# Optimization experiments

Measured on AMD Instinct MI355X. Metric: run time of the kernel, lower is better.

The kernel has to match this reference:

```python
import jax, jax.numpy as jnp
import numpy as np

ACT_BIT = 8
WEIGHT_BIT = 8
BIAS_BIT = 32
EPS = 1e-8


def _sym_scale(sat_max, bit):
    # symmetric_linear_quantization_params: scale = clamp(sat, 1e-8) / (2^(b-1)-1)
    n = 2 ** (bit - 1) - 1
    return jnp.maximum(sat_max, EPS) / n


def _sym_quant(x, scale, bit):
    # SymmetricQuantFunction: round(x/scale) clamped to [-2^(b-1), 2^(b-1)-1]
    n = 2 ** (bit - 1) - 1
    return jnp.clip(jnp.round(x / scale), -n - 1, n)


def setup_inputs() -> dict:
    key = jax.random.key(0)
    kx, kw, kb = jax.random.split(key, 3)
    B, S, D_IN, D_OUT = 4, 2048, 4096, 4096
    x = jax.random.normal(kx, (B, S, D_IN), dtype=jnp.float32)
    W = jax.random.normal(kw, (D_OUT, D_IN), dtype=jnp.float32) * 0.02
    b = jax.random.normal(kb, (D_OUT,), dtype=jnp.float32) * 0.02
    return {"x": x, "W": W, "b": b}


def reference(x, W, b):
    # --- QuantAct (per-tensor symmetric int8, min/max from x itself) ---
    x_min, x_max = x.min(), x.max()
    act_scale = _sym_scale(jnp.maximum(jnp.abs(x_min), jnp.abs(x_max)), ACT_BIT)
    x_int = _sym_quant(x, act_scale, ACT_BIT)  # [B,S,Din], int values in fp32

    # --- QuantLinearBase (per-tensor symmetric int8 weight, int32 bias) ---
    w_sat = jnp.maximum(jnp.abs(W.min()), jnp.abs(W.max()))
    w_scale = _sym_scale(w_sat, WEIGHT_BIT)
    w_int = _sym_quant(W, w_scale, WEIGHT_BIT)  # [Dout,Din]

    bias_scale = act_scale * w_scale
    n32 = 2 ** (BIAS_BIT - 1) - 1
    b_int = jnp.clip(jnp.round(b / bias_scale), -n32 - 1, n32)  # [Dout]

    # integer GEMM + bias, then rescale by act_scale * w_scale
    out_int = jnp.einsum("bsi,oi->bso", x_int, w_int) + b_int
    return out_int * bias_scale
```

## Files before the change

kernel.cpp:

```cpp
#include <hip/hip_runtime.h>
#include <cstdint>
#include <cstddef>


typedef int v4i __attribute__((ext_vector_type(4)));

__device__ __forceinline__ void async_copy16(const void* g, void* s) {
  __builtin_amdgcn_global_load_lds(
      (const __attribute__((address_space(1))) void*)g,
      (__attribute__((address_space(3))) void*)s, 16, 0, 0);
}

__device__ __forceinline__ float block_max(float m) {
  __shared__ float smax[4];
#pragma unroll
  for (int off = 32; off > 0; off >>= 1)
    m = fmaxf(m, __shfl_down(m, off, 64));
  if ((threadIdx.x & 63) == 0) smax[threadIdx.x >> 6] = m;
  __syncthreads();
  return fmaxf(fmaxf(smax[0], smax[1]), fmaxf(smax[2], smax[3]));
}

#define NBX 1024
#define NBW 512

__global__ __launch_bounds__(256) void absmax_partial_kernel(
    const float4* __restrict__ x, int xn4, const float4* __restrict__ w,
    int wn4, float* __restrict__ px, float* __restrict__ pw) {
  const float4* src;
  float* dst;
  int n4, bid, nb;
  if (blockIdx.x < NBX) {
    src = x; n4 = xn4; dst = px; bid = blockIdx.x; nb = NBX;
  } else {
    src = w; n4 = wn4; dst = pw; bid = blockIdx.x - NBX; nb = NBW;
  }
  float m = 0.0f;
  for (int i = bid * 256 + threadIdx.x; i < n4; i += nb * 256) {
    float4 v = src[i];
    m = fmaxf(m, fmaxf(fmaxf(fabsf(v.x), fabsf(v.y)),
                       fmaxf(fabsf(v.z), fabsf(v.w))));
  }
  m = block_max(m);
  if (threadIdx.x == 0) dst[bid] = m;
}

__global__ __launch_bounds__(256) void absmax_final_kernel(
    const float* __restrict__ px, const float* __restrict__ pw,
    float* __restrict__ sat) {
  const float* src = (blockIdx.x == 0) ? px : pw;
  const int n = (blockIdx.x == 0) ? NBX : NBW;
  float m = 0.0f;
  for (int i = threadIdx.x; i < n; i += 256) m = fmaxf(m, src[i]);
  m = block_max(m);
  if (threadIdx.x == 0) {
    sat[blockIdx.x] = m;
    sat[2 + blockIdx.x] = 127.0f / fmaxf(m, 1e-8f);
  }
}

__device__ __forceinline__ int pack4(float4 v, float inv) {
  int a = (int)fminf(fmaxf(rintf(v.x * inv), -128.0f), 127.0f);
  int b = (int)fminf(fmaxf(rintf(v.y * inv), -128.0f), 127.0f);
  int c = (int)fminf(fmaxf(rintf(v.z * inv), -128.0f), 127.0f);
  int d = (int)fminf(fmaxf(rintf(v.w * inv), -128.0f), 127.0f);
  return (a & 255) | ((b & 255) << 8) | ((c & 255) << 16) | ((d & 255) << 24);
}

#define QNB 2048

__global__ __launch_bounds__(256) void quant_fused_kernel(
    const float4* __restrict__ x, int xn16, const float4* __restrict__ w,
    int wn16, const float* __restrict__ sat, int4* __restrict__ xq,
    int4* __restrict__ wq) {
  const float invx = sat[2];
  const float invw = sat[3];
  const int nth = QNB * 256;
  const int t = blockIdx.x * 256 + threadIdx.x;
  for (int u = t; u < xn16; u += nth) {
    const float4* p = x + (size_t)u * 4;
    int4 o;
    o.x = pack4(p[0], invx);
    o.y = pack4(p[1], invx);
    o.z = pack4(p[2], invx);
    o.w = pack4(p[3], invx);
    xq[u] = o;
  }
  for (int u = t; u < wn16; u += nth) {
    const float4* p = w + (size_t)u * 4;
    int4 o;
    o.x = pack4(p[0], invw);
    o.y = pack4(p[1], invw);
    o.z = pack4(p[2], invw);
    o.w = pack4(p[3], invw);
    wq[u] = o;
  }
}

__global__ __launch_bounds__(256) void i8_gemm_kernel(
    const signed char* __restrict__ Aq, const signed char* __restrict__ Bq,
    const float* __restrict__ bias, const float* __restrict__ sat,
    float* __restrict__ out, int M, int N, int K) {
  __shared__ signed char Als[128 * 128];
  __shared__ signed char Bls[128 * 128];

  const int tid = threadIdx.x;
  const int lane = tid & 63;
  const int wave = tid >> 6;
  const int wm = (wave & 1) * 64;
  const int wn = (wave >> 1) * 64;

  const int nwg = gridDim.x * gridDim.y;
  int bid = blockIdx.y * gridDim.x + blockIdx.x;
  if ((nwg & 7) == 0) bid = (bid & 7) * (nwg >> 3) + (bid >> 3);
  const int N0 = (bid % gridDim.x) * 128;
  const int M0 = (bid / gridDim.x) * 128;

  const int srow = tid >> 3;
  const int sb = tid & 7;
  const int cg = sb ^ (srow & 7);
  const signed char* Ag = Aq + (size_t)(M0 + srow) * K + cg * 16;
  const signed char* Bg = Bq + (size_t)(N0 + srow) * K + cg * 16;
  signed char* AlsP = &Als[srow * 128 + sb * 16];
  signed char* BlsP = &Bls[srow * 128 + sb * 16];

  const int r15 = lane & 15;
  const int rx = r15 & 7;
  const int q4 = lane >> 4;
  const int kb0 = ((q4) ^ rx) * 16;
  const int kb1 = ((4 + q4) ^ rx) * 16;

  v4i acc[4][4] = {};

  for (int kt = 0; kt < K; kt += 128) {
    __syncthreads();
#pragma unroll
    for (int r = 0; r < 4; ++r) {
      async_copy16(Ag + kt + (size_t)(32 * r) * K, AlsP + 32 * r * 128);
      async_copy16(Bg + kt + (size_t)(32 * r) * K, BlsP + 32 * r * 128);
    }
    __syncthreads();

#pragma unroll
    for (int ks = 0; ks < 2; ++ks) {
      const int kb = ks ? kb1 : kb0;
      v4i af[4], bf[4];
#pragma unroll
      for (int t = 0; t < 4; ++t) {
        af[t] = *(const v4i*)&Als[(wm + t * 16 + r15) * 128 + kb];
        bf[t] = *(const v4i*)&Bls[(wn + t * 16 + r15) * 128 + kb];
      }
#pragma unroll
      for (int tm = 0; tm < 4; ++tm)
#pragma unroll
        for (int tn = 0; tn < 4; ++tn)
          acc[tm][tn] = __builtin_amdgcn_mfma_i32_16x16x64_i8(
              af[tm], bf[tn], acc[tm][tn], 0, 0, 0);
    }
  }

  const float act_s = fmaxf(sat[0], 1e-8f) / 127.0f;
  const float w_s = fmaxf(sat[1], 1e-8f) / 127.0f;
  const float bscale = act_s * w_s;

#pragma unroll
  for (int tn = 0; tn < 4; ++tn) {
    const int col = N0 + wn + tn * 16 + r15;
    const float fb = rintf(bias[col] / bscale);
#pragma unroll
    for (int tm = 0; tm < 4; ++tm) {
      const int row0 = M0 + wm + tm * 16 + q4 * 4;
#pragma unroll
      for (int r = 0; r < 4; ++r) {
        out[(size_t)(row0 + r) * N + col] =
            ((float)acc[tm][tn][r] + fb) * bscale;
      }
    }
  }
}

extern "C" void kernel_launch(void* const* d_in, const int* in_sizes, int n_in,
                              void* d_out, int out_size, void* d_ws,
                              size_t ws_size, hipStream_t stream) {
  const float* x = (const float*)d_in[0];
  const float* W = (const float*)d_in[1];
  const float* b = (const float*)d_in[2];
  float* out = (float*)d_out;

  const int Dout = in_sizes[2];
  const int K = in_sizes[1] / Dout;
  const int M = in_sizes[0] / K;
  const int N = Dout;

  float* sat = (float*)d_ws;
  float* px = sat + 16;
  float* pw = px + NBX;
  signed char* xq = (signed char*)d_ws + 8192;
  signed char* wq = xq + (size_t)M * K;

  const int xn4 = in_sizes[0] / 4;
  const int wn4 = in_sizes[1] / 4;

  absmax_partial_kernel<<<NBX + NBW, 256, 0, stream>>>(
      (const float4*)x, xn4, (const float4*)W, wn4, px, pw);
  absmax_final_kernel<<<2, 256, 0, stream>>>(px, pw, sat);
  quant_fused_kernel<<<QNB, 256, 0, stream>>>(
      (const float4*)x, xn4 / 4, (const float4*)W, wn4 / 4, sat, (int4*)xq,
      (int4*)wq);

  dim3 grid(N / 128, M / 128);
  i8_gemm_kernel<<<grid, 256, 0, stream>>>(xq, wq, b, sat, out, M, N, K);
}
```

Before: 493.1 us.

## Rewrite int8 GEMM with 256x256 tiles and 4-stage async LDS pipeline

The int8 GEMM moves from 128x128 tiles with 4 waves and a single-buffered load/compute loop to 256x256 tiles with 8 waves, a 4-deep ring of 64-wide K slices in LDS, and a rotation-based swizzle. Global-to-LDS copies for future tiles are interleaved between two MFMA phases, with explicit vmcnt waits, barriers and setprio, so memory latency overlaps with compute. This raises reuse per loaded byte and hides load latency. In exchange it uses 128KB of LDS and more accumulator registers, which limits occupancy to one block per CU.

```diff
diff --git a/kernel.cpp b/kernel.cpp
--- a/kernel.cpp
+++ b/kernel.cpp
@@ -97,66 +97,111 @@
   }
 }
 
-__global__ __launch_bounds__(256) void i8_gemm_kernel(
+__global__ __launch_bounds__(512, 2) void i8_gemm_kernel(
     const signed char* __restrict__ Aq, const signed char* __restrict__ Bq,
     const float* __restrict__ bias, const float* __restrict__ sat,
     float* __restrict__ out, int M, int N, int K) {
-  __shared__ signed char Als[128 * 128];
-  __shared__ signed char Bls[128 * 128];
+  __shared__ signed char lds[4][2][256 * 64];
 
   const int tid = threadIdx.x;
   const int lane = tid & 63;
-  const int wave = tid >> 6;
-  const int wm = (wave & 1) * 64;
-  const int wn = (wave >> 1) * 64;
+  const int wid = tid >> 6;
+  const int wr = wid >> 2;
+  const int wc = wid & 3;
+  const int r15 = lane & 15;
+  const int q4 = lane >> 4;
 
   const int nwg = gridDim.x * gridDim.y;
   int bid = blockIdx.y * gridDim.x + blockIdx.x;
   if ((nwg & 7) == 0) bid = (bid & 7) * (nwg >> 3) + (bid >> 3);
-  const int N0 = (bid % gridDim.x) * 128;
-  const int M0 = (bid / gridDim.x) * 128;
-
-  const int srow = tid >> 3;
-  const int sb = tid & 7;
-  const int cg = sb ^ (srow & 7);
+  const int N0 = (bid % gridDim.x) * 256;
+  const int M0 = (bid / gridDim.x) * 256;
+
+  const int srow = tid >> 2;
+  const int sb = tid & 3;
+  const int cg = (sb - ((srow >> 1) & 3)) & 3;
   const signed char* Ag = Aq + (size_t)(M0 + srow) * K + cg * 16;
   const signed char* Bg = Bq + (size_t)(N0 + srow) * K + cg * 16;
-  signed char* AlsP = &Als[srow * 128 + sb * 16];
-  signed char* BlsP = &Bls[srow * 128 + sb * 16];
-
-  const int r15 = lane & 15;
-  const int rx = r15 & 7;
-  const int q4 = lane >> 4;
-  const int kb0 = ((q4) ^ rx) * 16;
-  const int kb1 = ((4 + q4) ^ rx) * 16;
-
-  v4i acc[4][4] = {};
-
-  for (int kt = 0; kt < K; kt += 128) {
-    __syncthreads();
-#pragma unroll
-    for (int r = 0; r < 4; ++r) {
-      async_copy16(Ag + kt + (size_t)(32 * r) * K, AlsP + 32 * r * 128);
-      async_copy16(Bg + kt + (size_t)(32 * r) * K, BlsP + 32 * r * 128);
-    }
-    __syncthreads();
-
-#pragma unroll
-    for (int ks = 0; ks < 2; ++ks) {
-      const int kb = ks ? kb1 : kb0;
-      v4i af[4], bf[4];
-#pragma unroll
-      for (int t = 0; t < 4; ++t) {
-        af[t] = *(const v4i*)&Als[(wm + t * 16 + r15) * 128 + kb];
-        bf[t] = *(const v4i*)&Bls[(wn + t * 16 + r15) * 128 + kb];
-      }
-#pragma unroll
-      for (int tm = 0; tm < 4; ++tm)
-#pragma unroll
-        for (int tn = 0; tn < 4; ++tn)
-          acc[tm][tn] = __builtin_amdgcn_mfma_i32_16x16x64_i8(
-              af[tm], bf[tn], acc[tm][tn], 0, 0, 0);
-    }
+  const int d0 = srow * 64 + sb * 16;
+  const size_t rstep = (size_t)128 * K;
+
+  const int kboff = ((q4 + ((r15 >> 1) & 3)) & 3) * 16;
+
+  v4i acc[8][4] = {};
+  const int nt = K >> 6;
+
+  for (int T = 0; T < 3; ++T) {
+    const size_t ko = (size_t)T << 6;
+    signed char* bA = &lds[T & 3][0][0];
+    signed char* bB = &lds[T & 3][1][0];
+    async_copy16(Ag + ko, bA + d0);
+    async_copy16(Ag + ko + rstep, bA + d0 + 8192);
+    async_copy16(Bg + ko, bB + d0);
+    async_copy16(Bg + ko + rstep, bB + d0 + 8192);
+  }
+  asm volatile("s_waitcnt vmcnt(8)" ::: "memory");
+  __builtin_amdgcn_s_barrier();
+
+  for (int t = 0; t < nt; ++t) {
+    const signed char* bA = &lds[t & 3][0][0];
+    const signed char* bB = &lds[t & 3][1][0];
+    const int tp = t + 3;
+    const bool st = tp < nt;
+    signed char* sA = &lds[tp & 3][0][0];
+    signed char* sB = &lds[tp & 3][1][0];
+    const size_t ko = (size_t)tp << 6;
+
+    v4i af[4], bf[4];
+
+#pragma unroll
+    for (int f = 0; f < 4; ++f) {
+      af[f] = *(const v4i*)(bA + (wr * 128 + f * 16 + r15) * 64 + kboff);
+      bf[f] = *(const v4i*)(bB + (wc * 64 + f * 16 + r15) * 64 + kboff);
+    }
+    if (st) {
+      async_copy16(Ag + ko, sA + d0);
+      async_copy16(Ag + ko + rstep, sA + d0 + 8192);
+    }
+    __builtin_amdgcn_s_barrier();
+    asm volatile("s_waitcnt lgkmcnt(0)" ::: "memory");
+    __builtin_amdgcn_sched_barrier(0);
+    __builtin_amdgcn_s_setprio(1);
+#pragma unroll
+    for (int fm = 0; fm < 4; ++fm)
+#pragma unroll
+      for (int fn = 0; fn < 4; ++fn)
+        acc[fm][fn] = __builtin_amdgcn_mfma_i32_16x16x64_i8(
+            af[fm], bf[fn], acc[fm][fn], 0, 0, 0);
+    __builtin_amdgcn_s_setprio(0);
+    __builtin_amdgcn_s_barrier();
+
+#pragma unroll
+    for (int f = 0; f < 4; ++f) {
+      af[f] = *(const v4i*)(bA + (wr * 128 + 64 + f * 16 + r15) * 64 + kboff);
+    }
+    if (st) {
+      async_copy16(Bg + ko, sB + d0);
+      async_copy16(Bg + ko + rstep, sB + d0 + 8192);
+    }
+    __builtin_amdgcn_s_barrier();
+    asm volatile("s_waitcnt lgkmcnt(0)" ::: "memory");
+    __builtin_amdgcn_sched_barrier(0);
+    __builtin_amdgcn_s_setprio(1);
+#pragma unroll
+    for (int fm = 0; fm < 4; ++fm)
+#pragma unroll
+      for (int fn = 0; fn < 4; ++fn)
+        acc[4 + fm][fn] = __builtin_amdgcn_mfma_i32_16x16x64_i8(
+            af[fm], bf[fn], acc[4 + fm][fn], 0, 0, 0);
+    __builtin_amdgcn_s_setprio(0);
+    if (t < nt - 3) {
+      asm volatile("s_waitcnt vmcnt(8)" ::: "memory");
+    } else if (t == nt - 3) {
+      asm volatile("s_waitcnt vmcnt(4)" ::: "memory");
+    } else if (t == nt - 2) {
+      asm volatile("s_waitcnt vmcnt(0)" ::: "memory");
+    }
+    __builtin_amdgcn_s_barrier();
   }
 
   const float act_s = fmaxf(sat[0], 1e-8f) / 127.0f;
@@ -164,16 +209,16 @@
   const float bscale = act_s * w_s;
 
 #pragma unroll
-  for (int tn = 0; tn < 4; ++tn) {
-    const int col = N0 + wn + tn * 16 + r15;
+  for (int fn = 0; fn < 4; ++fn) {
+    const int col = N0 + wc * 64 + fn * 16 + r15;
     const float fb = rintf(bias[col] / bscale);
 #pragma unroll
-    for (int tm = 0; tm < 4; ++tm) {
-      const int row0 = M0 + wm + tm * 16 + q4 * 4;
-#pragma unroll
-      for (int r = 0; r < 4; ++r) {
-        out[(size_t)(row0 + r) * N + col] =
-            ((float)acc[tm][tn][r] + fb) * bscale;
+    for (int f = 0; f < 8; ++f) {
+      const int row0 = M0 + wr * 128 + f * 16 + q4 * 4;
+#pragma unroll
+      for (int rr = 0; rr < 4; ++rr) {
+        out[(size_t)(row0 + rr) * N + col] =
+            ((float)acc[f][fn][rr] + fb) * bscale;
       }
     }
   }
@@ -208,6 +253,6 @@
       (const float4*)x, xn4 / 4, (const float4*)W, wn4 / 4, sat, (int4*)xq,
       (int4*)wq);
 
-  dim3 grid(N / 128, M / 128);
-  i8_gemm_kernel<<<grid, 256, 0, stream>>>(xq, wq, b, sat, out, M, N, K);
-}
+  dim3 grid(N / 256, M / 256);
+  i8_gemm_kernel<<<grid, 512, 0, stream>>>(xq, wq, b, sat, out, M, N, K);
+}
```

New measurement: 438.2 us. -11.1%, faster.
